# Optimization experiments

Hardware: AMD Instinct MI355X
Metric: run time of the kernel (lower is better)

The kernel has to match this reference:

```python
import jax, jax.numpy as jnp
import numpy as np

N = 256
FEAT = 1024           # box_head.fc7.out_features
HID_REL = 256         # RelationProposalNetwork hidden_dim
GCN_HID = 256         # gcn_hidden
HEADS = 4
NUM_PARTS = 20
OUT = NUM_PARTS + 1
TOPK = 3
IN_GCN = FEAT + 4


def setup_inputs() -> dict:
    key = jax.random.key(0)
    ks = jax.random.split(key, 16)
    features = jax.random.normal(ks[0], (N, FEAT), jnp.float32)
    # valid pixel-space boxes (x1, y1, x2, y2) inside an 800x800 image
    xy = jax.random.uniform(ks[1], (N, 2), jnp.float32, 0.0, 700.0)
    wh = jax.random.uniform(ks[2], (N, 2), jnp.float32, 8.0, 100.0)
    boxes = jnp.concatenate([xy, xy + wh], axis=1)
    s = 0.02
    W_fc1 = jax.random.normal(ks[3], (2 * FEAT + 4, HID_REL), jnp.float32) * s
    b_fc1 = jnp.zeros((HID_REL,), jnp.float32)
    W_fc2 = jax.random.normal(ks[4], (HID_REL, 1), jnp.float32) * s
    b_fc2 = jnp.zeros((1,), jnp.float32)
    W1 = jax.random.normal(ks[5], (IN_GCN, HEADS * GCN_HID), jnp.float32) * s
    a_src1 = jax.random.normal(ks[6], (HEADS, GCN_HID), jnp.float32) * s
    a_dst1 = jax.random.normal(ks[7], (HEADS, GCN_HID), jnp.float32) * s
    b1 = jnp.zeros((HEADS * GCN_HID,), jnp.float32)
    W2 = jax.random.normal(ks[8], (HEADS * GCN_HID, OUT), jnp.float32) * s
    a_src2 = jax.random.normal(ks[9], (1, OUT), jnp.float32) * s
    a_dst2 = jax.random.normal(ks[10], (1, OUT), jnp.float32) * s
    b2 = jnp.zeros((OUT,), jnp.float32)
    return {
        "features": features, "boxes": boxes,
        "W_fc1": W_fc1, "b_fc1": b_fc1, "W_fc2": W_fc2, "b_fc2": b_fc2,
        "W1": W1, "a_src1": a_src1, "a_dst1": a_dst1, "b1": b1,
        "W2": W2, "a_src2": a_src2, "a_dst2": a_dst2, "b2": b2,
        "img_h": 800, "img_w": 800,
    }


def _gat_layer(x, W, a_src, a_dst, bias, s, t, n, heads, ch):
    # PyG GATConv: message flows edge_index[0] (s) -> edge_index[1] (t),
    # softmax over incoming edges of each target node t.
    h = (x @ W).reshape(n, heads, ch)                       # [n, H, C]
    e = jax.nn.leaky_relu(
        jnp.einsum("ehc,hc->eh", h[s], a_src)
        + jnp.einsum("ehc,hc->eh", h[t], a_dst), 0.2)        # [E, H]
    m = jnp.full((n, heads), -1e30, e.dtype).at[t].max(e)    # segment max
    p = jnp.exp(e - m[t])
    denom = jax.ops.segment_sum(p, t, num_segments=n)
    alpha = p / denom[t]                                     # [E, H]
    out = jax.ops.segment_sum(alpha[:, :, None] * h[s], t, num_segments=n)
    return out.reshape(n, heads * ch) + bias


def _forward(features, boxes, W_fc1, b_fc1, W_fc2, b_fc2,
             W1, a_src1, a_dst1, b1, W2, a_src2, a_dst2, b2, img_h, img_w):
    n = features.shape[0]
    # --- RelationProposalNetwork: dense O(N^2) pairwise MLP ---
    f1 = jnp.broadcast_to(features[:, None, :], (n, n, FEAT))
    f2 = jnp.broadcast_to(features[None, :, :], (n, n, FEAT))
    geom = jnp.abs(boxes[:, None, :] - boxes[None, :, :])    # [n, n, 4]
    pair = jnp.concatenate([f1, f2, geom], axis=-1)          # [n, n, 2052]
    hid = jax.nn.relu(pair @ W_fc1 + b_fc1)                  # [n, n, 256]
    rel = (hid @ W_fc2 + b_fc2)[..., 0]                      # [n, n]
    # --- top-k graph construction (drop first = self, as in source) ---
    idx = jax.lax.top_k(rel, TOPK + 1)[1][:, 1:]             # [n, topk]
    s_e = jnp.repeat(jnp.arange(n), TOPK)                    # edge_index[0]
    t_e = idx.reshape(-1)                                    # edge_index[1]
    loops = jnp.arange(n)                                    # GATConv add_self_loops
    s_e = jnp.concatenate([s_e, loops])
    t_e = jnp.concatenate([t_e, loops])
    # --- normalized box geometry node features ---
    scale = jnp.array([img_w, img_h, img_w, img_h], jnp.float32)
    nb = boxes / scale
    geomn = jnp.stack([nb[:, 0], nb[:, 1], nb[:, 2] - nb[:, 0], nb[:, 3] - nb[:, 1]], axis=1)
    gcn_in = jnp.concatenate([features, geomn], axis=1)      # [n, 1028]
    # --- AttentionalGCN: GAT(heads=4) -> ReLU -> GAT(heads=1) ---
    h1 = jax.nn.relu(_gat_layer(gcn_in, W1, a_src1, a_dst1, b1, s_e, t_e, n, HEADS, GCN_HID))
    logits = _gat_layer(h1, W2, a_src2, a_dst2, b2, s_e, t_e, n, 1, OUT)
    return logits


def reference(features, boxes, W_fc1, b_fc1, W_fc2, b_fc2,
              W1, a_src1, a_dst1, b1, W2, a_src2, a_dst2, b2, img_h, img_w):
    logits = _forward(features, boxes, W_fc1, b_fc1, W_fc2, b_fc2,
                      W1, a_src1, a_dst1, b1, W2, a_src2, a_dst2, b2, img_h, img_w)
    labels = jnp.argmax(logits, axis=1)
    return logits, labels
```

## Files before the change

kernel.cpp:

```cpp
#include <hip/hip_runtime.h>
#include <math.h>

#define NN 256
#define FEAT 1024
#define HIDR 256
#define GCNH 256
#define M1 1024
#define OUTC 21
#define MAXDEG (NN + 1)
#define KC 16
#define KCH (FEAT / KC)
#define RB 16
#define FCOLS 1536

__device__ __forceinline__ void st_wt4(float* p, float4 v) {
    union { float4 f; unsigned long long u[2]; } cv; cv.f = v;
    __hip_atomic_store((unsigned long long*)p, cv.u[0],
                       __ATOMIC_RELAXED, __HIP_MEMORY_SCOPE_AGENT);
    __hip_atomic_store((unsigned long long*)p + 1, cv.u[1],
                       __ATOMIC_RELAXED, __HIP_MEMORY_SCOPE_AGENT);
}
__device__ __forceinline__ void st_wtf(float* p, float v) {
    __hip_atomic_store((unsigned*)p, __float_as_uint(v),
                       __ATOMIC_RELAXED, __HIP_MEMORY_SCOPE_AGENT);
}
__device__ __forceinline__ void st_wti(int* p, int v) {
    __hip_atomic_store(p, v, __ATOMIC_RELAXED, __HIP_MEMORY_SCOPE_AGENT);
}

__global__ __launch_bounds__(256) void k_big(
        const float* __restrict__ feat, const float* __restrict__ Wfc1,
        const float* __restrict__ W1, float* __restrict__ P,
        unsigned* bar) {
    int id = blockIdx.x;
    if (id == 0 && threadIdx.x == 0)
        __hip_atomic_store(bar, 0u, __ATOMIC_RELAXED, __HIP_MEMORY_SCOPE_AGENT);
    int xcd = id & 7, slot = id >> 3;
    int g = xcd + 8 * (slot >> 4);
    int rg = slot & 15;
    int cgy = g >> 4, kc = g & 15;
    __shared__ float fS[RB][KCH];
    int tid = threadIdx.x;
    int r0 = rg * RB, k0 = kc * KCH;
    for (int x = tid; x < RB * KCH; x += 256) {
        int r = x >> 6, kk = x & (KCH - 1);
        fS[r][kk] = feat[(size_t)(r0 + r) * FEAT + k0 + kk];
    }
    __syncthreads();
    int gc = cgy * 512 + tid * 2;
    const float* pW;
    int ld;
    if (gc < 256)      { pW = Wfc1 + (size_t)k0 * HIDR + gc;                  ld = HIDR; }
    else if (gc < 512) { pW = Wfc1 + (size_t)(FEAT + k0) * HIDR + (gc - 256); ld = HIDR; }
    else               { pW = W1   + (size_t)k0 * M1 + (gc - 512);            ld = M1;   }
    float2 acc[RB];
#pragma unroll
    for (int r = 0; r < RB; r++) { acc[r].x = 0.f; acc[r].y = 0.f; }
    float2 w0 = *(const float2*)(pW);
    float2 w1 = *(const float2*)(pW + ld);
    float2 w2 = *(const float2*)(pW + 2 * ld);
    float2 w3 = *(const float2*)(pW + 3 * ld);
    for (int kk = 0; kk < KCH; kk += 4) {
        pW += 4 * ld;
        float2 n0 = *(const float2*)(pW);
        float2 n1 = *(const float2*)(pW + ld);
        float2 n2 = *(const float2*)(pW + 2 * ld);
        float2 n3 = *(const float2*)(pW + 3 * ld);
#pragma unroll
        for (int r = 0; r < RB; r++) {
            float4 f = *(const float4*)&fS[r][kk];
            acc[r].x = fmaf(f.x, w0.x, acc[r].x); acc[r].y = fmaf(f.x, w0.y, acc[r].y);
            acc[r].x = fmaf(f.y, w1.x, acc[r].x); acc[r].y = fmaf(f.y, w1.y, acc[r].y);
            acc[r].x = fmaf(f.z, w2.x, acc[r].x); acc[r].y = fmaf(f.z, w2.y, acc[r].y);
            acc[r].x = fmaf(f.w, w3.x, acc[r].x); acc[r].y = fmaf(f.w, w3.y, acc[r].y);
        }
        w0 = n0; w1 = n1; w2 = n2; w3 = n3;
    }
    float* Pp = P + ((size_t)r0 * KC + kc) * FCOLS + gc;
#pragma unroll
    for (int r = 0; r < RB; r++)
        *(float2*)(Pp + (size_t)r * KC * FCOLS) = acc[r];
}

__device__ __forceinline__ void gsync(unsigned* bar, unsigned expected) {
    __syncthreads();
    if (threadIdx.x == 0) {
        __hip_atomic_fetch_add(bar, 1u, __ATOMIC_RELAXED,
                               __HIP_MEMORY_SCOPE_AGENT);
        while (__hip_atomic_load(bar, __ATOMIC_RELAXED,
                                 __HIP_MEMORY_SCOPE_AGENT) < expected)
            __builtin_amdgcn_s_sleep(1);
    }
    __syncthreads();
    __builtin_amdgcn_fence(__ATOMIC_ACQUIRE, "workgroup");
}

__global__ __launch_bounds__(512, 4) void k_fused(
        const float* __restrict__ P, const float* __restrict__ bfc1,
        const float* __restrict__ boxes, const int* __restrict__ imh,
        const int* __restrict__ imw, const float* __restrict__ W1,
        const float* __restrict__ as1, const float* __restrict__ ad1,
        const float* __restrict__ Wfc1, const float* __restrict__ Wfc2,
        const float* __restrict__ b1, const float* __restrict__ W2,
        const float* __restrict__ as2, const float* __restrict__ ad2,
        const float* __restrict__ b2,
        float* __restrict__ BT4, float* __restrict__ hpre,
        float* __restrict__ es1, float* __restrict__ ed1,
        int* __restrict__ idxTop, float* __restrict__ h2,
        float* __restrict__ es2, float* __restrict__ ed2,
        unsigned* bar, float* __restrict__ out) {
    __shared__ float gS[4];
    __shared__ float As[HIDR];
    __shared__ float sval[512];
    __shared__ unsigned long long swk[8];
    __shared__ int win;
    __shared__ int pfxw[4];
    __shared__ int lst[MAXDEG];
    __shared__ int dgS;
    __shared__ float sc[MAXDEG * 4];
    __shared__ float sh[M1];
    __shared__ float part[24 * OUTC];
    __shared__ float h2row[OUTC];
    __shared__ float scD[MAXDEG];
    __shared__ float lv[OUTC];

    int row = blockIdx.x, tid = threadIdx.x;

    int c4 = tid * 4;
    bool actA = (tid < 384);
    float4 s4;
    if (actA) {
        const float* p = P + (size_t)row * (KC * FCOLS) + c4;
        float4 a0 = *(const float4*)(p);
        float4 a1 = *(const float4*)(p + FCOLS);
        float4 a2 = *(const float4*)(p + 2 * FCOLS);
        float4 a3 = *(const float4*)(p + 3 * FCOLS);
#pragma unroll
        for (int q = 4; q < KC; q += 4) {
            float4 t0 = *(const float4*)(p + (size_t)q * FCOLS);
            float4 t1 = *(const float4*)(p + (size_t)(q + 1) * FCOLS);
            float4 t2 = *(const float4*)(p + (size_t)(q + 2) * FCOLS);
            float4 t3 = *(const float4*)(p + (size_t)(q + 3) * FCOLS);
            a0.x += t0.x; a0.y += t0.y; a0.z += t0.z; a0.w += t0.w;
            a1.x += t1.x; a1.y += t1.y; a1.z += t1.z; a1.w += t1.w;
            a2.x += t2.x; a2.y += t2.y; a2.z += t2.z; a2.w += t2.w;
            a3.x += t3.x; a3.y += t3.y; a3.z += t3.z; a3.w += t3.w;
        }
        s4.x = (a0.x + a1.x) + (a2.x + a3.x);
        s4.y = (a0.y + a1.y) + (a2.y + a3.y);
        s4.z = (a0.z + a1.z) + (a2.z + a3.z);
        s4.w = (a0.w + a1.w) + (a2.w + a3.w);
    }
    if (tid == 0) {
        float w = (float)imw[0], h = (float)imh[0];
        float x1 = boxes[row * 4 + 0] / w, y1 = boxes[row * 4 + 1] / h;
        float x2 = boxes[row * 4 + 2] / w, y2 = boxes[row * 4 + 3] / h;
        gS[0] = x1; gS[1] = y1; gS[2] = x2 - x1; gS[3] = y2 - y1;
    }
    __syncthreads();
    if (actA) {
        if (c4 < 256) {
            float4 bv = *(const float4*)(bfc1 + c4);
            s4.x += bv.x; s4.y += bv.y; s4.z += bv.z; s4.w += bv.w;
            *(float4*)(&As[c4]) = s4;
        } else if (c4 < 512) {
            int kk = c4 - 256;
            st_wt4(BT4 + (size_t)(kk >> 2) * (NN * 4) + row * 4, s4);
        } else {
            int ch = c4 - 512;
            float g0 = gS[0], g1 = gS[1], g2 = gS[2], g3 = gS[3];
            float4 wv;
            wv = *(const float4*)(W1 + (size_t)(FEAT + 0) * M1 + ch);
            s4.x = fmaf(g0, wv.x, s4.x); s4.y = fmaf(g0, wv.y, s4.y);
            s4.z = fmaf(g0, wv.z, s4.z); s4.w = fmaf(g0, wv.w, s4.w);
            wv = *(const float4*)(W1 + (size_t)(FEAT + 1) * M1 + ch);
            s4.x = fmaf(g1, wv.x, s4.x); s4.y = fmaf(g1, wv.y, s4.y);
            s4.z = fmaf(g1, wv.z, s4.z); s4.w = fmaf(g1, wv.w, s4.w);
            wv = *(const float4*)(W1 + (size_t)(FEAT + 2) * M1 + ch);
            s4.x = fmaf(g2, wv.x, s4.x); s4.y = fmaf(g2, wv.y, s4.y);
            s4.z = fmaf(g2, wv.z, s4.z); s4.w = fmaf(g2, wv.w, s4.w);
            wv = *(const float4*)(W1 + (size_t)(FEAT + 3) * M1 + ch);
            s4.x = fmaf(g3, wv.x, s4.x); s4.y = fmaf(g3, wv.y, s4.y);
            s4.z = fmaf(g3, wv.z, s4.z); s4.w = fmaf(g3, wv.w, s4.w);
            st_wt4(hpre + (size_t)row * M1 + ch, s4);
            float4 a = *(const float4*)(as1 + ch);
            float4 bv = *(const float4*)(ad1 + ch);
            float ps = s4.x * a.x + s4.y * a.y + s4.z * a.z + s4.w * a.w;
            float pd = s4.x * bv.x + s4.y * bv.y + s4.z * bv.z + s4.w * bv.w;
#pragma unroll
            for (int o = 32; o > 0; o >>= 1) {
                ps += __shfl_down(ps, o);
                pd += __shfl_down(pd, o);
            }
            if ((tid & 63) == 0) {
                int head = (tid - 128) >> 6;
                st_wtf(es1 + row * 4 + head, ps);
                st_wtf(ed1 + row * 4 + head, pd);
            }
        }
    }
    int j = tid & 255;
    float bi0 = boxes[row * 4 + 0], bi1 = boxes[row * 4 + 1];
    float bi2 = boxes[row * 4 + 2], bi3 = boxes[row * 4 + 3];
    float g0 = fabsf(bi0 - boxes[j * 4 + 0]);
    float g1 = fabsf(bi1 - boxes[j * 4 + 1]);
    float g2 = fabsf(bi2 - boxes[j * 4 + 2]);
    float g3 = fabsf(bi3 - boxes[j * 4 + 3]);

    gsync(bar, NN);

    {
        int half = __builtin_amdgcn_readfirstlane(tid >> 8);
        int k0 = half * 128;
        const float* pB  = BT4 + (size_t)(k0 >> 2) * (NN * 4) + j * 4;
        const float* pA  = As + k0;
        const float* pW2 = Wfc2 + k0;
        const float* pg0 = Wfc1 + (size_t)(2 * FEAT + 0) * HIDR + k0;
        const float* pg1 = Wfc1 + (size_t)(2 * FEAT + 1) * HIDR + k0;
        const float* pg2 = Wfc1 + (size_t)(2 * FEAT + 2) * HIDR + k0;
        const float* pg3 = Wfc1 + (size_t)(2 * FEAT + 3) * HIDR + k0;
        float acc = 0.f;
#pragma unroll 4
        for (int kk = 0; kk < 128; kk += 4) {
            float4 a4 = *(const float4*)(pA + kk);
            float4 w4 = *(const float4*)(pW2 + kk);
            float4 q0 = *(const float4*)(pg0 + kk);
            float4 q1 = *(const float4*)(pg1 + kk);
            float4 q2 = *(const float4*)(pg2 + kk);
            float4 q3 = *(const float4*)(pg3 + kk);
            float4 b4 = *(const float4*)pB;
            pB += NN * 4;
            float v;
            v = a4.x + b4.x; v = fmaf(g0, q0.x, v); v = fmaf(g1, q1.x, v);
            v = fmaf(g2, q2.x, v); v = fmaf(g3, q3.x, v);
            acc = fmaf(fmaxf(v, 0.f), w4.x, acc);
            v = a4.y + b4.y; v = fmaf(g0, q0.y, v); v = fmaf(g1, q1.y, v);
            v = fmaf(g2, q2.y, v); v = fmaf(g3, q3.y, v);
            acc = fmaf(fmaxf(v, 0.f), w4.y, acc);
            v = a4.z + b4.z; v = fmaf(g0, q0.z, v); v = fmaf(g1, q1.z, v);
            v = fmaf(g2, q2.z, v); v = fmaf(g3, q3.z, v);
            acc = fmaf(fmaxf(v, 0.f), w4.z, acc);
            v = a4.w + b4.w; v = fmaf(g0, q0.w, v); v = fmaf(g1, q1.w, v);
            v = fmaf(g2, q2.w, v); v = fmaf(g3, q3.w, v);
            acc = fmaf(fmaxf(v, 0.f), w4.w, acc);
        }
        sval[tid] = acc;
    }
    __syncthreads();
    if (tid < 256) sval[tid] = sval[tid] + sval[tid + 256];
    __syncthreads();
    for (int r = 0; r < 4; r++) {
        unsigned long long key = 0ULL;
        if (tid < 256) {
            unsigned u = __float_as_uint(sval[tid]);
            u = (u & 0x80000000u) ? ~u : (u | 0x80000000u);
            key = ((unsigned long long)u << 32) | (unsigned)(NN - 1 - tid);
        }
#pragma unroll
        for (int o = 32; o > 0; o >>= 1) {
            unsigned long long nk = __shfl_down(key, o);
            if (nk > key) key = nk;
        }
        if ((tid & 63) == 0) swk[tid >> 6] = key;
        __syncthreads();
        if (tid == 0) {
            unsigned long long m = swk[0];
#pragma unroll
            for (int q = 1; q < 8; q++) if (swk[q] > m) m = swk[q];
            int wj = NN - 1 - (int)(m & 0xFFFFFFFFu);
            win = wj;
            if (r > 0) st_wti(idxTop + row * 3 + (r - 1), wj);
        }
        __syncthreads();
        if (tid == win) sval[tid] = -1e38f;
        __syncthreads();
    }

    gsync(bar, 2 * NN);

    int f = 0;
    if (tid < 256)
        f = (idxTop[tid * 3 + 0] == row) | (idxTop[tid * 3 + 1] == row)
          | (idxTop[tid * 3 + 2] == row);
    unsigned long long bm = __ballot(f);
    int lane = tid & 63, wv6 = tid >> 6;
    int rank = __popcll(bm & ((1ULL << lane) - 1ULL));
    if (tid < 256 && lane == 0) pfxw[wv6] = __popcll(bm);
    __syncthreads();
    {
        int base = 0;
#pragma unroll
        for (int w = 0; w < 4; w++) base += (w < wv6) ? pfxw[w] : 0;
        if (tid < 256 && f) lst[base + rank] = tid;
    }
    if (tid == 0) {
        int tot = pfxw[0] + pfxw[1] + pfxw[2] + pfxw[3];
        lst[tot] = row;
        dgS = tot + 1;
    }
    __syncthreads();
    int dg = dgS;
    for (int p = tid; p < dg * 4; p += 512) {
        int e = p >> 2, hq2 = p & 3;
        int s = lst[e];
        float v = es1[s * 4 + hq2] + ed1[row * 4 + hq2];
        sc[p] = v >= 0.f ? v : 0.2f * v;
    }
    __syncthreads();
    int hq = tid & 3;
    {
        float lm = -1e30f;
        for (int e = tid >> 2; e < dg; e += 128)
            lm = fmaxf(lm, sc[e * 4 + hq]);
#pragma unroll
        for (int o = 4; o <= 32; o <<= 1) lm = fmaxf(lm, __shfl_xor(lm, o));
        if (lane < 4) sval[wv6 * 4 + hq] = lm;
        __syncthreads();
        float m = sval[hq];
#pragma unroll
        for (int w = 1; w < 8; w++) m = fmaxf(m, sval[w * 4 + hq]);
        float ls = 0.f;
        for (int e = tid >> 2; e < dg; e += 128) {
            float pv = expf(sc[e * 4 + hq] - m);
            sc[e * 4 + hq] = pv;
            ls += pv;
        }
#pragma unroll
        for (int o = 4; o <= 32; o <<= 1) ls += __shfl_xor(ls, o);
        if (lane < 4) sval[32 + wv6 * 4 + hq] = ls;
        __syncthreads();
        float den = sval[32 + hq];
#pragma unroll
        for (int w = 1; w < 8; w++) den += sval[32 + w * 4 + hq];
        for (int e = tid >> 2; e < dg; e += 128)
            sc[e * 4 + hq] = sc[e * 4 + hq] / den;
    }
    __syncthreads();
    {
        int col = tid & 255, hh = (tid >> 8) * 2;
        float acc0 = 0.f, acc1 = 0.f;
        int e = 0;
        for (; e + 8 <= dg; e += 8) {
            float v0[8], v1[8];
#pragma unroll
            for (int u = 0; u < 8; u++) {
                const float* hs = hpre + (size_t)lst[e + u] * M1;
                v0[u] = hs[hh * GCNH + col];
                v1[u] = hs[(hh + 1) * GCNH + col];
            }
#pragma unroll
            for (int u = 0; u < 8; u++) {
                acc0 = fmaf(sc[(e + u) * 4 + hh],     v0[u], acc0);
                acc1 = fmaf(sc[(e + u) * 4 + hh + 1], v1[u], acc1);
            }
        }
        for (; e < dg; e++) {
            const float* hs = hpre + (size_t)lst[e] * M1;
            acc0 = fmaf(sc[e * 4 + hh],     hs[hh * GCNH + col],       acc0);
            acc1 = fmaf(sc[e * 4 + hh + 1], hs[(hh + 1) * GCNH + col], acc1);
        }
        int c0 = hh * GCNH + col, c1 = (hh + 1) * GCNH + col;
        sh[c0] = fmaxf(acc0 + b1[c0], 0.f);
        sh[c1] = fmaxf(acc1 + b1[c1], 0.f);
    }
    __syncthreads();
    if (tid < 504) {
        int o = tid % OUTC, pq = tid / OUTC;
        float a2 = 0.f;
        for (int d = pq; d < M1; d += 24)
            a2 = fmaf(sh[d], W2[d * OUTC + o], a2);
        part[pq * OUTC + o] = a2;
    }
    __syncthreads();
    if (tid < OUTC) {
        float ssum = 0.f;
        for (int pq = 0; pq < 24; pq++) ssum += part[pq * OUTC + tid];
        st_wtf(h2 + row * OUTC + tid, ssum);
        h2row[tid] = ssum;
    }
    __syncthreads();
    if (tid == 0) {
        float ssum = 0.f, dd = 0.f;
        for (int k = 0; k < OUTC; k++) {
            ssum = fmaf(h2row[k], as2[k], ssum);
            dd = fmaf(h2row[k], ad2[k], dd);
        }
        st_wtf(es2 + row, ssum);
        st_wtf(ed2 + row, dd);
    }

    gsync(bar, 3 * NN);

    int dgT = dgS;
    float edt = ed2[row];
    for (int p = tid; p < dgT; p += 512) {
        int s = lst[p];
        float v = es2[s] + edt;
        scD[p] = v >= 0.f ? v : 0.2f * v;
    }
    __syncthreads();
    {
        float lm = -1e30f;
        for (int p = tid; p < dgT; p += 512) lm = fmaxf(lm, scD[p]);
#pragma unroll
        for (int o = 1; o <= 32; o <<= 1) lm = fmaxf(lm, __shfl_xor(lm, o));
        if (lane == 0) sval[wv6] = lm;
        __syncthreads();
        float m = sval[0];
#pragma unroll
        for (int w = 1; w < 8; w++) m = fmaxf(m, sval[w]);
        float ls = 0.f;
        for (int p = tid; p < dgT; p += 512) {
            float pv = expf(scD[p] - m);
            scD[p] = pv;
            ls += pv;
        }
#pragma unroll
        for (int o = 1; o <= 32; o <<= 1) ls += __shfl_xor(ls, o);
        if (lane == 0) sval[8 + wv6] = ls;
        __syncthreads();
        float den = sval[8];
#pragma unroll
        for (int w = 1; w < 8; w++) den += sval[8 + w];
        __syncthreads();
        if (tid < 504) {
            int o = tid % OUTC, eg = tid / OUTC;
            float acc = 0.f;
            for (int e = eg; e < dgT; e += 24) {
                int s = lst[e];
                acc = fmaf(scD[e], h2[(size_t)s * OUTC + o], acc);
            }
            part[eg * OUTC + o] = acc;
        }
        __syncthreads();
        if (tid < OUTC) {
            float ssum = 0.f;
            for (int eg = 0; eg < 24; eg++) ssum += part[eg * OUTC + tid];
            float v = ssum / den + b2[tid];
            out[row * OUTC + tid] = v;
            lv[tid] = v;
        }
    }
    __syncthreads();
    if (tid == 0) {
        int best = 0;
        float bv = lv[0];
        for (int o = 1; o < OUTC; o++)
            if (lv[o] > bv) { bv = lv[o]; best = o; }
        out[NN * OUTC + row] = (float)best;
    }
}

extern "C" void kernel_launch(void* const* d_in, const int* in_sizes, int n_in,
                              void* d_out, int out_size, void* d_ws,
                              size_t ws_size, hipStream_t stream) {
    const float* feat  = (const float*)d_in[0];
    const float* boxes = (const float*)d_in[1];
    const float* Wfc1  = (const float*)d_in[2];
    const float* bfc1  = (const float*)d_in[3];
    const float* Wfc2  = (const float*)d_in[4];
    const float* bfc2  = (const float*)d_in[5];   (void)bfc2;
    const float* W1    = (const float*)d_in[6];
    const float* as1   = (const float*)d_in[7];
    const float* ad1   = (const float*)d_in[8];
    const float* b1    = (const float*)d_in[9];
    const float* W2    = (const float*)d_in[10];
    const float* as2   = (const float*)d_in[11];
    const float* ad2   = (const float*)d_in[12];
    const float* b2    = (const float*)d_in[13];
    const int*   imh   = (const int*)d_in[14];
    const int*   imw   = (const int*)d_in[15];

    float* ws = (float*)d_ws;
    float* P     = ws;  ws += KC * NN * FCOLS;
    float* BT4   = ws;  ws += NN * HIDR;
    float* hpre  = ws;  ws += NN * M1;
    float* es1   = ws;  ws += NN * 4;
    float* ed1   = ws;  ws += NN * 4;
    float* h2    = ws;  ws += NN * OUTC;
    float* es2   = ws;  ws += NN;
    float* ed2   = ws;  ws += NN;
    int* idxTop  = (int*)ws;
    unsigned* bar = (unsigned*)(idxTop + NN * 3);

    float* out = (float*)d_out;

    k_big<<<768, 256, 0, stream>>>(feat, Wfc1, W1, P, bar);
    k_fused<<<NN, 512, 0, stream>>>(P, bfc1, boxes, imh, imw, W1, as1, ad1,
                                    Wfc1, Wfc2, b1, W2, as2, ad2, b2,
                                    BT4, hpre, es1, ed1, idxTop,
                                    h2, es2, ed2, bar, out);
}
```

Baseline: 150.3 us.

## Split persistent fused kernel into four stage kernels replacing grid barriers

Replaces the single persistent kernel, which used atomic spin-wait grid barriers between stages, with four separate kernel launches (stA, stB, stC, stD) ordered on the stream. State that was kept in shared memory across stages (the A row, the incoming-edge list and the degree) now goes through global workspace buffers. The aim is to drop the spin-barrier cost and let each stage use its own block size and shared memory footprint. The cost is extra launch overhead and additional global-memory traffic between stages.

```diff
diff --git a/kernel.cpp b/kernel.cpp
--- a/kernel.cpp
+++ b/kernel.cpp
@@ -13,28 +13,11 @@
 #define RB 16
 #define FCOLS 1536
 
-__device__ __forceinline__ void st_wt4(float* p, float4 v) {
-    union { float4 f; unsigned long long u[2]; } cv; cv.f = v;
-    __hip_atomic_store((unsigned long long*)p, cv.u[0],
-                       __ATOMIC_RELAXED, __HIP_MEMORY_SCOPE_AGENT);
-    __hip_atomic_store((unsigned long long*)p + 1, cv.u[1],
-                       __ATOMIC_RELAXED, __HIP_MEMORY_SCOPE_AGENT);
-}
-__device__ __forceinline__ void st_wtf(float* p, float v) {
-    __hip_atomic_store((unsigned*)p, __float_as_uint(v),
-                       __ATOMIC_RELAXED, __HIP_MEMORY_SCOPE_AGENT);
-}
-__device__ __forceinline__ void st_wti(int* p, int v) {
-    __hip_atomic_store(p, v, __ATOMIC_RELAXED, __HIP_MEMORY_SCOPE_AGENT);
-}
 
 __global__ __launch_bounds__(256) void k_big(
         const float* __restrict__ feat, const float* __restrict__ Wfc1,
-        const float* __restrict__ W1, float* __restrict__ P,
-        unsigned* bar) {
+        const float* __restrict__ W1, float* __restrict__ P) {
     int id = blockIdx.x;
-    if (id == 0 && threadIdx.x == 0)
-        __hip_atomic_store(bar, 0u, __ATOMIC_RELAXED, __HIP_MEMORY_SCOPE_AGENT);
     int xcd = id & 7, slot = id >> 3;
     int g = xcd + 8 * (slot >> 4);
     int rg = slot & 15;
@@ -82,75 +65,38 @@
         *(float2*)(Pp + (size_t)r * KC * FCOLS) = acc[r];
 }
 
-__device__ __forceinline__ void gsync(unsigned* bar, unsigned expected) {
-    __syncthreads();
-    if (threadIdx.x == 0) {
-        __hip_atomic_fetch_add(bar, 1u, __ATOMIC_RELAXED,
-                               __HIP_MEMORY_SCOPE_AGENT);
-        while (__hip_atomic_load(bar, __ATOMIC_RELAXED,
-                                 __HIP_MEMORY_SCOPE_AGENT) < expected)
-            __builtin_amdgcn_s_sleep(1);
-    }
-    __syncthreads();
-    __builtin_amdgcn_fence(__ATOMIC_ACQUIRE, "workgroup");
-}
-
-__global__ __launch_bounds__(512, 4) void k_fused(
+__global__ __launch_bounds__(384) void k_stA(
         const float* __restrict__ P, const float* __restrict__ bfc1,
         const float* __restrict__ boxes, const int* __restrict__ imh,
         const int* __restrict__ imw, const float* __restrict__ W1,
         const float* __restrict__ as1, const float* __restrict__ ad1,
-        const float* __restrict__ Wfc1, const float* __restrict__ Wfc2,
-        const float* __restrict__ b1, const float* __restrict__ W2,
-        const float* __restrict__ as2, const float* __restrict__ ad2,
-        const float* __restrict__ b2,
-        float* __restrict__ BT4, float* __restrict__ hpre,
-        float* __restrict__ es1, float* __restrict__ ed1,
-        int* __restrict__ idxTop, float* __restrict__ h2,
-        float* __restrict__ es2, float* __restrict__ ed2,
-        unsigned* bar, float* __restrict__ out) {
+        float* __restrict__ A, float* __restrict__ BT4,
+        float* __restrict__ hpre, float* __restrict__ es1,
+        float* __restrict__ ed1) {
     __shared__ float gS[4];
-    __shared__ float As[HIDR];
-    __shared__ float sval[512];
-    __shared__ unsigned long long swk[8];
-    __shared__ int win;
-    __shared__ int pfxw[4];
-    __shared__ int lst[MAXDEG];
-    __shared__ int dgS;
-    __shared__ float sc[MAXDEG * 4];
-    __shared__ float sh[M1];
-    __shared__ float part[24 * OUTC];
-    __shared__ float h2row[OUTC];
-    __shared__ float scD[MAXDEG];
-    __shared__ float lv[OUTC];
-
     int row = blockIdx.x, tid = threadIdx.x;
-
     int c4 = tid * 4;
-    bool actA = (tid < 384);
+    const float* p = P + (size_t)row * (KC * FCOLS) + c4;
+    float4 a0 = *(const float4*)(p);
+    float4 a1 = *(const float4*)(p + FCOLS);
+    float4 a2 = *(const float4*)(p + 2 * FCOLS);
+    float4 a3 = *(const float4*)(p + 3 * FCOLS);
+#pragma unroll
+    for (int q = 4; q < KC; q += 4) {
+        float4 t0 = *(const float4*)(p + (size_t)q * FCOLS);
+        float4 t1 = *(const float4*)(p + (size_t)(q + 1) * FCOLS);
+        float4 t2 = *(const float4*)(p + (size_t)(q + 2) * FCOLS);
+        float4 t3 = *(const float4*)(p + (size_t)(q + 3) * FCOLS);
+        a0.x += t0.x; a0.y += t0.y; a0.z += t0.z; a0.w += t0.w;
+        a1.x += t1.x; a1.y += t1.y; a1.z += t1.z; a1.w += t1.w;
+        a2.x += t2.x; a2.y += t2.y; a2.z += t2.z; a2.w += t2.w;
+        a3.x += t3.x; a3.y += t3.y; a3.z += t3.z; a3.w += t3.w;
+    }
     float4 s4;
-    if (actA) {
-        const float* p = P + (size_t)row * (KC * FCOLS) + c4;
-        float4 a0 = *(const float4*)(p);
-        float4 a1 = *(const float4*)(p + FCOLS);
-        float4 a2 = *(const float4*)(p + 2 * FCOLS);
-        float4 a3 = *(const float4*)(p + 3 * FCOLS);
-#pragma unroll
-        for (int q = 4; q < KC; q += 4) {
-            float4 t0 = *(const float4*)(p + (size_t)q * FCOLS);
-            float4 t1 = *(const float4*)(p + (size_t)(q + 1) * FCOLS);
-            float4 t2 = *(const float4*)(p + (size_t)(q + 2) * FCOLS);
-            float4 t3 = *(const float4*)(p + (size_t)(q + 3) * FCOLS);
-            a0.x += t0.x; a0.y += t0.y; a0.z += t0.z; a0.w += t0.w;
-            a1.x += t1.x; a1.y += t1.y; a1.z += t1.z; a1.w += t1.w;
-            a2.x += t2.x; a2.y += t2.y; a2.z += t2.z; a2.w += t2.w;
-            a3.x += t3.x; a3.y += t3.y; a3.z += t3.z; a3.w += t3.w;
-        }
-        s4.x = (a0.x + a1.x) + (a2.x + a3.x);
-        s4.y = (a0.y + a1.y) + (a2.y + a3.y);
-        s4.z = (a0.z + a1.z) + (a2.z + a3.z);
-        s4.w = (a0.w + a1.w) + (a2.w + a3.w);
-    }
+    s4.x = (a0.x + a1.x) + (a2.x + a3.x);
+    s4.y = (a0.y + a1.y) + (a2.y + a3.y);
+    s4.z = (a0.z + a1.z) + (a2.z + a3.z);
+    s4.w = (a0.w + a1.w) + (a2.w + a3.w);
     if (tid == 0) {
         float w = (float)imw[0], h = (float)imh[0];
         float x1 = boxes[row * 4 + 0] / w, y1 = boxes[row * 4 + 1] / h;
@@ -158,47 +104,57 @@
         gS[0] = x1; gS[1] = y1; gS[2] = x2 - x1; gS[3] = y2 - y1;
     }
     __syncthreads();
-    if (actA) {
-        if (c4 < 256) {
-            float4 bv = *(const float4*)(bfc1 + c4);
-            s4.x += bv.x; s4.y += bv.y; s4.z += bv.z; s4.w += bv.w;
-            *(float4*)(&As[c4]) = s4;
-        } else if (c4 < 512) {
-            int kk = c4 - 256;
-            st_wt4(BT4 + (size_t)(kk >> 2) * (NN * 4) + row * 4, s4);
-        } else {
-            int ch = c4 - 512;
-            float g0 = gS[0], g1 = gS[1], g2 = gS[2], g3 = gS[3];
-            float4 wv;
-            wv = *(const float4*)(W1 + (size_t)(FEAT + 0) * M1 + ch);
-            s4.x = fmaf(g0, wv.x, s4.x); s4.y = fmaf(g0, wv.y, s4.y);
-            s4.z = fmaf(g0, wv.z, s4.z); s4.w = fmaf(g0, wv.w, s4.w);
-            wv = *(const float4*)(W1 + (size_t)(FEAT + 1) * M1 + ch);
-            s4.x = fmaf(g1, wv.x, s4.x); s4.y = fmaf(g1, wv.y, s4.y);
-            s4.z = fmaf(g1, wv.z, s4.z); s4.w = fmaf(g1, wv.w, s4.w);
-            wv = *(const float4*)(W1 + (size_t)(FEAT + 2) * M1 + ch);
-            s4.x = fmaf(g2, wv.x, s4.x); s4.y = fmaf(g2, wv.y, s4.y);
-            s4.z = fmaf(g2, wv.z, s4.z); s4.w = fmaf(g2, wv.w, s4.w);
-            wv = *(const float4*)(W1 + (size_t)(FEAT + 3) * M1 + ch);
-            s4.x = fmaf(g3, wv.x, s4.x); s4.y = fmaf(g3, wv.y, s4.y);
-            s4.z = fmaf(g3, wv.z, s4.z); s4.w = fmaf(g3, wv.w, s4.w);
-            st_wt4(hpre + (size_t)row * M1 + ch, s4);
-            float4 a = *(const float4*)(as1 + ch);
-            float4 bv = *(const float4*)(ad1 + ch);
-            float ps = s4.x * a.x + s4.y * a.y + s4.z * a.z + s4.w * a.w;
-            float pd = s4.x * bv.x + s4.y * bv.y + s4.z * bv.z + s4.w * bv.w;
-#pragma unroll
-            for (int o = 32; o > 0; o >>= 1) {
-                ps += __shfl_down(ps, o);
-                pd += __shfl_down(pd, o);
-            }
-            if ((tid & 63) == 0) {
-                int head = (tid - 128) >> 6;
-                st_wtf(es1 + row * 4 + head, ps);
-                st_wtf(ed1 + row * 4 + head, pd);
-            }
-        }
-    }
+    if (c4 < 256) {
+        float4 bv = *(const float4*)(bfc1 + c4);
+        s4.x += bv.x; s4.y += bv.y; s4.z += bv.z; s4.w += bv.w;
+        *(float4*)(A + (size_t)row * HIDR + c4) = s4;
+    } else if (c4 < 512) {
+        int kk = c4 - 256;
+        *(float4*)(BT4 + (size_t)(kk >> 2) * (NN * 4) + row * 4) = s4;
+    } else {
+        int ch = c4 - 512;
+        float g0 = gS[0], g1 = gS[1], g2 = gS[2], g3 = gS[3];
+        float4 wv;
+        wv = *(const float4*)(W1 + (size_t)(FEAT + 0) * M1 + ch);
+        s4.x = fmaf(g0, wv.x, s4.x); s4.y = fmaf(g0, wv.y, s4.y);
+        s4.z = fmaf(g0, wv.z, s4.z); s4.w = fmaf(g0, wv.w, s4.w);
+        wv = *(const float4*)(W1 + (size_t)(FEAT + 1) * M1 + ch);
+        s4.x = fmaf(g1, wv.x, s4.x); s4.y = fmaf(g1, wv.y, s4.y);
+        s4.z = fmaf(g1, wv.z, s4.z); s4.w = fmaf(g1, wv.w, s4.w);
+        wv = *(const float4*)(W1 + (size_t)(FEAT + 2) * M1 + ch);
+        s4.x = fmaf(g2, wv.x, s4.x); s4.y = fmaf(g2, wv.y, s4.y);
+        s4.z = fmaf(g2, wv.z, s4.z); s4.w = fmaf(g2, wv.w, s4.w);
+        wv = *(const float4*)(W1 + (size_t)(FEAT + 3) * M1 + ch);
+        s4.x = fmaf(g3, wv.x, s4.x); s4.y = fmaf(g3, wv.y, s4.y);
+        s4.z = fmaf(g3, wv.z, s4.z); s4.w = fmaf(g3, wv.w, s4.w);
+        *(float4*)(hpre + (size_t)row * M1 + ch) = s4;
+        float4 a = *(const float4*)(as1 + ch);
+        float4 bv = *(const float4*)(ad1 + ch);
+        float ps = s4.x * a.x + s4.y * a.y + s4.z * a.z + s4.w * a.w;
+        float pd = s4.x * bv.x + s4.y * bv.y + s4.z * bv.z + s4.w * bv.w;
+#pragma unroll
+        for (int o = 32; o > 0; o >>= 1) {
+            ps += __shfl_down(ps, o);
+            pd += __shfl_down(pd, o);
+        }
+        if ((tid & 63) == 0) {
+            int head = (tid - 128) >> 6;
+            es1[row * 4 + head] = ps;
+            ed1[row * 4 + head] = pd;
+        }
+    }
+}
+
+__global__ __launch_bounds__(512) void k_stB(
+        const float* __restrict__ A, const float* __restrict__ boxes,
+        const float* __restrict__ Wfc1, const float* __restrict__ Wfc2,
+        const float* __restrict__ BT4, int* __restrict__ idxTop) {
+    __shared__ float As[HIDR];
+    __shared__ float sval[512];
+    __shared__ unsigned long long swk[8];
+    __shared__ int win;
+    int row = blockIdx.x, tid = threadIdx.x;
+    if (tid < 256) As[tid] = A[(size_t)row * HIDR + tid];
     int j = tid & 255;
     float bi0 = boxes[row * 4 + 0], bi1 = boxes[row * 4 + 1];
     float bi2 = boxes[row * 4 + 2], bi3 = boxes[row * 4 + 3];
@@ -206,9 +162,7 @@
     float g1 = fabsf(bi1 - boxes[j * 4 + 1]);
     float g2 = fabsf(bi2 - boxes[j * 4 + 2]);
     float g3 = fabsf(bi3 - boxes[j * 4 + 3]);
-
-    gsync(bar, NN);
-
+    __syncthreads();
     {
         int half = __builtin_amdgcn_readfirstlane(tid >> 8);
         int k0 = half * 128;
@@ -269,15 +223,31 @@
             for (int q = 1; q < 8; q++) if (swk[q] > m) m = swk[q];
             int wj = NN - 1 - (int)(m & 0xFFFFFFFFu);
             win = wj;
-            if (r > 0) st_wti(idxTop + row * 3 + (r - 1), wj);
+            if (r > 0) idxTop[row * 3 + (r - 1)] = wj;
         }
         __syncthreads();
         if (tid == win) sval[tid] = -1e38f;
         __syncthreads();
     }
-
-    gsync(bar, 2 * NN);
-
+}
+
+__global__ __launch_bounds__(512) void k_stC(
+        const int* __restrict__ idxTop, const float* __restrict__ es1,
+        const float* __restrict__ ed1, const float* __restrict__ hpre,
+        const float* __restrict__ b1, const float* __restrict__ W2,
+        const float* __restrict__ as2, const float* __restrict__ ad2,
+        int* __restrict__ deg, int* __restrict__ inlist,
+        float* __restrict__ h2, float* __restrict__ es2,
+        float* __restrict__ ed2) {
+    __shared__ float sval[512];
+    __shared__ int pfxw[4];
+    __shared__ int lst[MAXDEG];
+    __shared__ int dgS;
+    __shared__ float sc[MAXDEG * 4];
+    __shared__ float sh[M1];
+    __shared__ float part[24 * OUTC];
+    __shared__ float h2row[OUTC];
+    int row = blockIdx.x, tid = threadIdx.x;
     int f = 0;
     if (tid < 256)
         f = (idxTop[tid * 3 + 0] == row) | (idxTop[tid * 3 + 1] == row)
@@ -291,12 +261,17 @@
         int base = 0;
 #pragma unroll
         for (int w = 0; w < 4; w++) base += (w < wv6) ? pfxw[w] : 0;
-        if (tid < 256 && f) lst[base + rank] = tid;
+        if (tid < 256 && f) {
+            lst[base + rank] = tid;
+            inlist[row * MAXDEG + base + rank] = tid;
+        }
     }
     if (tid == 0) {
         int tot = pfxw[0] + pfxw[1] + pfxw[2] + pfxw[3];
         lst[tot] = row;
+        inlist[row * MAXDEG + tot] = row;
         dgS = tot + 1;
+        deg[row] = tot + 1;
     }
     __syncthreads();
     int dg = dgS;
@@ -375,7 +350,7 @@
     if (tid < OUTC) {
         float ssum = 0.f;
         for (int pq = 0; pq < 24; pq++) ssum += part[pq * OUTC + tid];
-        st_wtf(h2 + row * OUTC + tid, ssum);
+        h2[row * OUTC + tid] = ssum;
         h2row[tid] = ssum;
     }
     __syncthreads();
@@ -385,16 +360,28 @@
             ssum = fmaf(h2row[k], as2[k], ssum);
             dd = fmaf(h2row[k], ad2[k], dd);
         }
-        st_wtf(es2 + row, ssum);
-        st_wtf(ed2 + row, dd);
-    }
-
-    gsync(bar, 3 * NN);
-
-    int dgT = dgS;
+        es2[row] = ssum;
+        ed2[row] = dd;
+    }
+}
+
+__global__ __launch_bounds__(512) void k_stD(
+        const int* __restrict__ deg, const int* __restrict__ inlist,
+        const float* __restrict__ es2, const float* __restrict__ ed2,
+        const float* __restrict__ h2, const float* __restrict__ b2,
+        float* __restrict__ out) {
+    __shared__ float sval[512];
+    __shared__ int lst[MAXDEG];
+    __shared__ float scD[MAXDEG];
+    __shared__ float part[24 * OUTC];
+    __shared__ float lv[OUTC];
+    int row = blockIdx.x, tid = threadIdx.x;
+    int lane = tid & 63, wv6 = tid >> 6;
+    int dgT = deg[row];
     float edt = ed2[row];
     for (int p = tid; p < dgT; p += 512) {
-        int s = lst[p];
+        int s = inlist[row * MAXDEG + p];
+        lst[p] = s;
         float v = es2[s] + edt;
         scD[p] = v >= 0.f ? v : 0.2f * v;
     }
@@ -473,6 +460,7 @@
 
     float* ws = (float*)d_ws;
     float* P     = ws;  ws += KC * NN * FCOLS;
+    float* A     = ws;  ws += NN * HIDR;
     float* BT4   = ws;  ws += NN * HIDR;
     float* hpre  = ws;  ws += NN * M1;
     float* es1   = ws;  ws += NN * 4;
@@ -481,13 +469,16 @@
     float* es2   = ws;  ws += NN;
     float* ed2   = ws;  ws += NN;
     int* idxTop  = (int*)ws;
-    unsigned* bar = (unsigned*)(idxTop + NN * 3);
+    int* deg     = idxTop + NN * 3;
+    int* inlist  = deg + NN;
 
     float* out = (float*)d_out;
 
-    k_big<<<768, 256, 0, stream>>>(feat, Wfc1, W1, P, bar);
-    k_fused<<<NN, 512, 0, stream>>>(P, bfc1, boxes, imh, imw, W1, as1, ad1,
-                                    Wfc1, Wfc2, b1, W2, as2, ad2, b2,
-                                    BT4, hpre, es1, ed1, idxTop,
-                                    h2, es2, ed2, bar, out);
-}
+    k_big<<<768, 256, 0, stream>>>(feat, Wfc1, W1, P);
+    k_stA<<<NN, 384, 0, stream>>>(P, bfc1, boxes, imh, imw, W1, as1, ad1,
+                                  A, BT4, hpre, es1, ed1);
+    k_stB<<<NN, 512, 0, stream>>>(A, boxes, Wfc1, Wfc2, BT4, idxTop);
+    k_stC<<<NN, 512, 0, stream>>>(idxTop, es1, ed1, hpre, b1, W2, as2, ad2,
+                                  deg, inlist, h2, es2, ed2);
+    k_stD<<<NN, 512, 0, stream>>>(deg, inlist, es2, ed2, h2, b2, out);
+}
```

Result: faster. 141.7 us (-5.7%).
